# Performance work log

Measured on AMD Instinct MI355X. Metric: run time of the kernel, lower is better.

The kernel has to match this reference:

```python
import jax, jax.numpy as jnp
import numpy as np

D_MODEL = 768
NUM_HEADS = 12
NUM_REG = 4
EPS = 1e-5


def _layernorm(x, g, b):
    mu = jnp.mean(x, axis=-1, keepdims=True)
    var = jnp.mean(jnp.square(x - mu), axis=-1, keepdims=True)
    return (x - mu) * jax.lax.rsqrt(var + EPS) * g + b


def _make_mask(seq_len):
    # True = masked (disallowed), matching torch attn_mask bool semantics.
    r1 = 1 + NUM_REG
    mask = np.ones((seq_len, seq_len), dtype=bool)
    mask[0, :] = False                      # context token attends to all
    mask[1:r1, :] = False                   # register tokens attend to all
    mask[r1:, :r1] = False                  # (not use_input_context_token) == False
    mask[r1:, r1:] = ~np.eye(seq_len - r1, dtype=bool)  # feature tokens: self only
    return jnp.asarray(mask)


def setup_inputs() -> dict:
    key = jax.random.key(0)
    ks = jax.random.split(key, 16)
    B, C, H, W = 8, D_MODEL, 32, 32
    d = D_MODEL
    s = 0.02
    inp = {
        "x": jax.random.normal(ks[0], (B, C, H, W), jnp.float32),
        "context_token": jax.random.normal(ks[1], (B, 1, d), jnp.float32),
        "register_tokens": jax.random.normal(ks[2], (B, NUM_REG, d), jnp.float32),
        "in_proj_w": jax.random.normal(ks[3], (3 * d, d), jnp.float32) * s,
        "in_proj_b": jnp.zeros((3 * d,), jnp.float32),
        "out_w": jax.random.normal(ks[4], (d, d), jnp.float32) * s,
        "out_b": jnp.zeros((d,), jnp.float32),
        "ln1_g": jnp.ones((d,), jnp.float32),
        "ln1_b": jnp.zeros((d,), jnp.float32),
        "ln2_g": jnp.ones((d,), jnp.float32),
        "ln2_b": jnp.zeros((d,), jnp.float32),
        "w1": jax.random.normal(ks[5], (4 * d, d), jnp.float32) * s,
        "b1": jnp.zeros((4 * d,), jnp.float32),
        "w2": jax.random.normal(ks[6], (d, 4 * d), jnp.float32) * s,
        "b2": jnp.zeros((d,), jnp.float32),
    }
    return inp


def reference(x, context_token, register_tokens, in_proj_w, in_proj_b,
              out_w, out_b, ln1_g, ln1_b, ln2_g, ln2_b, w1, b1, w2, b2):
    B, C, H, W = x.shape
    d, nh = D_MODEL, NUM_HEADS
    hd = d // nh
    x_flat = x.reshape(B, C, H * W).transpose(0, 2, 1)          # [B, HW, d]
    tokens = jnp.concatenate([context_token, register_tokens], axis=1)
    xw = _layernorm(jnp.concatenate([tokens, x_flat], axis=1), ln1_g, ln1_b)  # [B, S, d]
    S = xw.shape[1]

    qkv = xw @ in_proj_w.T + in_proj_b                           # [B, S, 3d]
    q, k, v = jnp.split(qkv, 3, axis=-1)
    q = q.reshape(B, S, nh, hd).transpose(0, 2, 1, 3)            # [B, nh, S, hd]
    k = k.reshape(B, S, nh, hd).transpose(0, 2, 1, 3)
    v = v.reshape(B, S, nh, hd).transpose(0, 2, 1, 3)

    scores = jnp.einsum("bhqd,bhkd->bhqk", q, k) / jnp.sqrt(jnp.float32(hd))
    mask = _make_mask(S)
    scores = jnp.where(mask, jnp.float32(-1e9), scores)
    probs = jax.nn.softmax(scores, axis=-1)
    attn = jnp.einsum("bhqk,bhkd->bhqd", probs, v)               # [B, nh, S, hd]
    attn = attn.transpose(0, 2, 1, 3).reshape(B, S, d)
    attn = attn @ out_w.T + out_b

    h1 = attn + xw                                                # residual
    ff = _layernorm(h1, ln2_g, ln2_b)
    ff = jax.nn.gelu(ff @ w1.T + b1, approximate=False) @ w2.T + b2
    out = ff + h1                                                 # [B, S, d]

    r1 = 1 + NUM_REG
    ctx_out = out[:, 0:1, :]
    reg_out = out[:, 1:r1, :]
    feat_out = out[:, r1:, :].transpose(0, 2, 1).reshape(B, C, H, W)
    return feat_out, ctx_out, reg_out
```

## Files before the change

kernel.cpp:

```cpp
#include <hip/hip_runtime.h>
#include <math.h>
#include <stdint.h>

#define SEQ 1029
#define BATCH 8
#define M_TOT (BATCH * SEQ)
#define M_PAD 8320
#define NCHUNK 17

typedef float floatx4 __attribute__((ext_vector_type(4)));
typedef __bf16 bf16x8 __attribute__((ext_vector_type(8)));

__device__ __forceinline__ unsigned short f2bf(float f) {
  union { float f; unsigned u; } v; v.f = f;
  unsigned r = v.u + 0x7fffu + ((v.u >> 16) & 1u);
  return (unsigned short)(r >> 16);
}
__device__ __forceinline__ float bf2f(unsigned short h) {
  union { unsigned u; float f; } v; v.u = ((unsigned)h) << 16;
  return v.f;
}
__device__ __forceinline__ float bf_lo(unsigned u) { union { unsigned x; float f; } v; v.x = u << 16; return v.f; }
__device__ __forceinline__ float bf_hi(unsigned u) { union { unsigned x; float f; } v; v.x = u & 0xffff0000u; return v.f; }

__device__ __forceinline__ float wave_sum(float v) {
#pragma unroll
  for (int off = 32; off > 0; off >>= 1) v += __shfl_xor(v, off, 64);
  return v;
}
__device__ __forceinline__ float wave_max(float v) {
#pragma unroll
  for (int off = 32; off > 0; off >>= 1) v = fmaxf(v, __shfl_xor(v, off, 64));
  return v;
}

__device__ __forceinline__ void gload16(const unsigned short* g, unsigned short* l) {
  __builtin_amdgcn_global_load_lds(
      (const __attribute__((address_space(1))) unsigned int*)g,
      (__attribute__((address_space(3))) unsigned int*)l, 16, 0, 0);
}

#define NQ_QKV 442368
#define NQ_OUT 147456
#define NQ_W1  589824
#define NQ_W2  589824
#define NQ_PAD 8448
__global__ void convert_all(const float4* __restrict__ inw, const float4* __restrict__ outw,
                            const float4* __restrict__ w1, const float4* __restrict__ w2,
                            ushort4* __restrict__ wqkv, ushort4* __restrict__ wout,
                            ushort4* __restrict__ w1b, ushort4* __restrict__ w2b,
                            ushort4* __restrict__ xw_pad, ushort4* __restrict__ attn_pad) {
  const int i = blockIdx.x * 256 + threadIdx.x;
  const float4* src; ushort4* dst; int off;
  if (i < NQ_QKV) { src = inw; dst = wqkv; off = i; }
  else if (i < NQ_QKV + NQ_OUT) { src = outw; dst = wout; off = i - NQ_QKV; }
  else if (i < NQ_QKV + NQ_OUT + NQ_W1) { src = w1; dst = w1b; off = i - NQ_QKV - NQ_OUT; }
  else if (i < NQ_QKV + NQ_OUT + NQ_W1 + NQ_W2) { src = w2; dst = w2b; off = i - NQ_QKV - NQ_OUT - NQ_W1; }
  else {
    const int j = i - (NQ_QKV + NQ_OUT + NQ_W1 + NQ_W2);
    const ushort4 z = {0, 0, 0, 0};
    if (j < NQ_PAD) { xw_pad[j] = z; attn_pad[j] = z; }
    return;
  }
  const float4 v = src[off];
  ushort4 o;
  o.x = f2bf(v.x); o.y = f2bf(v.y); o.z = f2bf(v.z); o.w = f2bf(v.w);
  dst[off] = o;
}
#define NQ_ALL (NQ_QKV + NQ_OUT + NQ_W1 + NQ_W2 + NQ_PAD)

__global__ __launch_bounds__(256) void ln1_feat(const float* __restrict__ x,
                                                const float* __restrict__ g,
                                                const float* __restrict__ bta,
                                                unsigned short* __restrict__ xw) {
  __shared__ float tile[768 * 17];
  const int b = blockIdx.y;
  const int hw0 = blockIdx.x * 16;
  const int t = threadIdx.x;
  const float* xb = x + (size_t)b * 768 * 1024;
  const int cl = t >> 4, hl = t & 15;
  for (int it = 0; it < 48; it++) {
    const int c = it * 16 + cl;
    tile[c * 17 + hl] = xb[(size_t)c * 1024 + hw0 + hl];
  }
  __syncthreads();
  const int wave = t >> 6, lane = t & 63;
  for (int tk = wave; tk < 16; tk += 4) {
    float vals[12], s = 0.f, ss = 0.f;
#pragma unroll
    for (int i = 0; i < 12; i++) {
      const float v = tile[(lane + 64 * i) * 17 + tk];
      vals[i] = v; s += v; ss += v * v;
    }
    s = wave_sum(s); ss = wave_sum(ss);
    const float mu = s * (1.0f / 768.0f);
    const float var = ss * (1.0f / 768.0f) - mu * mu;
    const float rs = rsqrtf(var + 1e-5f);
    const int row = b * SEQ + 5 + hw0 + tk;
    unsigned short* orow = xw + (size_t)row * 768;
#pragma unroll
    for (int i = 0; i < 12; i++) {
      const int c = lane + 64 * i;
      orow[c] = f2bf((vals[i] - mu) * rs * g[c] + bta[c]);
    }
  }
}

__global__ __launch_bounds__(256) void ln1_special(const float* __restrict__ ctx,
                                                   const float* __restrict__ regs,
                                                   const float* __restrict__ g,
                                                   const float* __restrict__ bta,
                                                   unsigned short* __restrict__ xw) {
  const int gw = blockIdx.x * 4 + (threadIdx.x >> 6);
  const int lane = threadIdx.x & 63;
  if (gw >= 40) return;
  const int b = gw / 5, s = gw % 5;
  const float* src = (s == 0) ? (ctx + (size_t)b * 768)
                              : (regs + ((size_t)b * 4 + (s - 1)) * 768);
  float vals[12], sm = 0.f, ss = 0.f;
#pragma unroll
  for (int i = 0; i < 12; i++) {
    const float v = src[lane + 64 * i];
    vals[i] = v; sm += v; ss += v * v;
  }
  sm = wave_sum(sm); ss = wave_sum(ss);
  const float mu = sm * (1.0f / 768.0f);
  const float var = ss * (1.0f / 768.0f) - mu * mu;
  const float rs = rsqrtf(var + 1e-5f);
  unsigned short* orow = xw + (size_t)(b * SEQ + s) * 768;
#pragma unroll
  for (int i = 0; i < 12; i++) {
    const int c = lane + 64 * i;
    orow[c] = f2bf((vals[i] - mu) * rs * g[c] + bta[c]);
  }
}

#define BM 128
#define BN 128
#define BK 32

template <int EPI, int K, int N>
__global__ __launch_bounds__(256, 4) void gemm_bt(const unsigned short* __restrict__ A,
                                                  const unsigned short* __restrict__ W,
                                                  const float* __restrict__ bias,
                                                  const unsigned short* __restrict__ residb,
                                                  const float* __restrict__ residf,
                                                  float* __restrict__ outf,
                                                  unsigned short* __restrict__ outb) {
  __shared__ alignas(16) unsigned short As[2][BM * BK];
  __shared__ alignas(16) unsigned short Ws[2][BN * BK];
  const int t = threadIdx.x;
  const int wave = t >> 6, lane = t & 63;
  const int quad = lane >> 4, l16 = lane & 15;
  const int wm = (wave & 1) * 64, wn = (wave >> 1) * 64;
  const int tileM = blockIdx.y * BM, tileN = blockIdx.x * BN;

  const int rl = lane >> 2;
  const int kc8 = ((lane & 3) ^ ((rl >> 1) & 3)) * 8;
  const unsigned short* Ag = A + (size_t)(tileM + wave * 16 + rl) * K;
  const unsigned short* Wg = W + (size_t)(tileN + wave * 16 + rl) * K;
  const int ldst = wave * 512 + lane * 8;

  const int koff = ((quad ^ ((l16 >> 1) & 3)) * 8);

  const floatx4 zero4 = {0.f, 0.f, 0.f, 0.f};
  floatx4 acc[4][4];
#pragma unroll
  for (int i = 0; i < 4; i++)
#pragma unroll
    for (int j = 0; j < 4; j++) acc[i][j] = zero4;

  auto dma = [&](int k0, int buf) {
    gload16(Ag + k0 + kc8, &As[buf][0] + ldst);
    gload16(Ag + (size_t)64 * K + k0 + kc8, &As[buf][0] + ldst + 2048);
    gload16(Wg + k0 + kc8, &Ws[buf][0] + ldst);
    gload16(Wg + (size_t)64 * K + k0 + kc8, &Ws[buf][0] + ldst + 2048);
  };
  auto compute = [&](int buf) {
    bf16x8 af[4], wf[4];
#pragma unroll
    for (int i = 0; i < 4; i++)
      af[i] = *(const bf16x8*)(&As[buf][0] + (wm + i * 16 + l16) * BK + koff);
#pragma unroll
    for (int j = 0; j < 4; j++)
      wf[j] = *(const bf16x8*)(&Ws[buf][0] + (wn + j * 16 + l16) * BK + koff);
#pragma unroll
    for (int i = 0; i < 4; i++)
#pragma unroll
      for (int j = 0; j < 4; j++)
        acc[i][j] = __builtin_amdgcn_mfma_f32_16x16x32_bf16(af[i], wf[j], acc[i][j], 0, 0, 0);
  };

  dma(0, 0);
#pragma unroll 1
  for (int k0 = 0; k0 < K; k0 += 2 * BK) {
    __syncthreads();
    if (k0 + BK < K) dma(k0 + BK, 1);
    compute(0);
    __syncthreads();
    if (k0 + 2 * BK < K) dma(k0 + 2 * BK, 0);
    compute(1);
  }

#pragma unroll
  for (int i = 0; i < 4; i++) {
    const int mbase = tileM + wm + i * 16 + quad * 4;
#pragma unroll
    for (int j = 0; j < 4; j++) {
      const int n = tileN + wn + j * 16 + l16;
      const float bv = bias[n];
#pragma unroll
      for (int r = 0; r < 4; r++) {
        const size_t idx = (size_t)(mbase + r) * N + n;
        float v = acc[i][j][r] + bv;
        if constexpr (EPI == 0) {
          outb[idx] = f2bf(v);
        } else if constexpr (EPI == 1) {
          outf[idx] = v + bf2f(residb[idx]);
        } else if constexpr (EPI == 2) {
          v = 0.5f * v * (1.0f + erff(v * 0.70710678118654752f));
          outb[idx] = f2bf(v);
        } else {
          outf[idx] = v + residf[idx];
        }
      }
    }
  }
}

__global__ __launch_bounds__(256) void attn_feat(const unsigned short* __restrict__ qkv,
                                                 unsigned short* __restrict__ attn) {
  __shared__ float kk[5][64];
  __shared__ float vv[5][64];
  const int b = blockIdx.z, h = blockIdx.y;
  const int t = threadIdx.x;
  const size_t base = (size_t)b * SEQ;
  for (int i = t; i < 320; i += 256) {
    const int j = i >> 6, dd = i & 63;
    const size_t rb = (base + j) * 2304 + (size_t)h * 64 + dd;
    kk[j][dd] = bf2f(qkv[rb + 768]);
    vv[j][dd] = bf2f(qkv[rb + 1536]);
  }
  __syncthreads();
  const int wave = t >> 6, lane = t & 63;
  const int s = 5 + blockIdx.x * 4 + wave;
  const size_t row = (base + s) * 2304 + (size_t)h * 64;
  const float q = bf2f(qkv[row + lane]);
  const float kself = bf2f(qkv[row + 768 + lane]);
  const float vself = bf2f(qkv[row + 1536 + lane]);
  float sc[6];
#pragma unroll
  for (int j = 0; j < 5; j++) sc[j] = wave_sum(q * kk[j][lane]) * 0.125f;
  sc[5] = wave_sum(q * kself) * 0.125f;
  float mx = sc[0];
#pragma unroll
  for (int j = 1; j < 6; j++) mx = fmaxf(mx, sc[j]);
  float den = 0.f, e[6];
#pragma unroll
  for (int j = 0; j < 6; j++) { e[j] = expf(sc[j] - mx); den += e[j]; }
  const float inv = 1.0f / den;
  float o = 0.f;
#pragma unroll
  for (int j = 0; j < 5; j++) o += e[j] * vv[j][lane];
  o += e[5] * vself;
  attn[(base + s) * 768 + (size_t)h * 64 + lane] = f2bf(o * inv);
}

__global__ __launch_bounds__(256) void attn_part(const unsigned short* __restrict__ qkv,
                                                 float* __restrict__ part) {
  __shared__ float qs[5][64];
  __shared__ float sc[5][64];
  __shared__ float mArr[5], lArr[5];
  __shared__ float og[4][320];
  const int c = blockIdx.x, h = blockIdx.y, b = blockIdx.z;
  const int t = threadIdx.x;
  const size_t base = (size_t)b * SEQ;
  const int kbase = (c < 16) ? (5 + 64 * c) : 0;
  const int nvalid = (c < 16) ? 64 : 5;

  for (int i = t; i < 320; i += 256)
    qs[i >> 6][i & 63] = bf2f(qkv[(base + (i >> 6)) * 2304 + (size_t)h * 64 + (i & 63)]);
  __syncthreads();

  const int keyloc = t >> 2, dc = t & 3;
  const int key = kbase + keyloc;
  const unsigned short* krow = qkv + (base + key) * 2304 + 768 + (size_t)h * 64;
  const uint4 k0 = *(const uint4*)(krow + dc * 8);
  const uint4 k1 = *(const uint4*)(krow + dc * 8 + 32);
  float kf[16];
  {
    const unsigned ku[8] = {k0.x, k0.y, k0.z, k0.w, k1.x, k1.y, k1.z, k1.w};
#pragma unroll
    for (int j = 0; j < 8; j++) { kf[2 * j] = bf_lo(ku[j]); kf[2 * j + 1] = bf_hi(ku[j]); }
  }
#pragma unroll
  for (int q = 0; q < 5; q++) {
    const float* qp = qs[q];
    float d0 = 0.f;
#pragma unroll
    for (int j = 0; j < 8; j++) d0 += qp[dc * 8 + j] * kf[j];
#pragma unroll
    for (int j = 0; j < 8; j++) d0 += qp[dc * 8 + 32 + j] * kf[8 + j];
    d0 += __shfl_xor(d0, 1, 64);
    d0 += __shfl_xor(d0, 2, 64);
    if (dc == 0) sc[q][keyloc] = (keyloc < nvalid) ? d0 * 0.125f : -1e30f;
  }
  __syncthreads();

  const int wave = t >> 6, lane = t & 63;
  for (int q = wave; q < 5; q += 4) {
    const float v = sc[q][lane];
    const float m = wave_max(v);
    const float e = expf(v - m);
    sc[q][lane] = e;
    const float l = wave_sum(e);
    if (lane == 0) { mArr[q] = m; lArr[q] = l; }
  }
  __syncthreads();

  const int d = t & 63, g = t >> 6;
  float o[5] = {0.f, 0.f, 0.f, 0.f, 0.f};
  for (int i = 0; i < 16; i++) {
    const int kl = g * 16 + i;
    const float v = bf2f(qkv[(base + kbase + kl) * 2304 + 1536 + (size_t)h * 64 + d]);
#pragma unroll
    for (int q = 0; q < 5; q++) o[q] += sc[q][kl] * v;
  }
#pragma unroll
  for (int q = 0; q < 5; q++) og[g][q * 64 + d] = o[q];
  __syncthreads();

  float* pw = part + (size_t)((b * 12 + h) * NCHUNK + c) * 5 * 66;
  for (int i = t; i < 320; i += 256) {
    const int q = i >> 6, dd = i & 63;
    pw[q * 66 + 2 + dd] = og[0][i] + og[1][i] + og[2][i] + og[3][i];
    if (dd == 0) { pw[q * 66] = mArr[q]; pw[q * 66 + 1] = lArr[q]; }
  }
}

__global__ __launch_bounds__(64) void attn_comb(const float* __restrict__ part,
                                                unsigned short* __restrict__ attn) {
  const int qi = blockIdx.x, h = blockIdx.y, b = blockIdx.z;
  const int d = threadIdx.x;
  float M = -3e38f, L = 0.f, o = 0.f;
  for (int c = 0; c < NCHUNK; c++) {
    const float* p = part + ((size_t)((b * 12 + h) * NCHUNK + c) * 5 + qi) * 66;
    const float mc = p[0], lc = p[1], oc = p[2 + d];
    if (mc > M) {
      const float s = expf(M - mc);
      L = L * s + lc; o = o * s + oc; M = mc;
    } else {
      const float w = expf(mc - M);
      L += lc * w; o += oc * w;
    }
  }
  attn[((size_t)b * SEQ + qi) * 768 + (size_t)h * 64 + d] = f2bf(o / L);
}

__global__ __launch_bounds__(256) void ln2_kernel(const float* __restrict__ h1,
                                                  const float* __restrict__ g,
                                                  const float* __restrict__ bta,
                                                  unsigned short* __restrict__ out) {
  const int row = blockIdx.x * 4 + (threadIdx.x >> 6);
  const int lane = threadIdx.x & 63;
  const float* r = h1 + (size_t)row * 768;
  float vals[12], sm = 0.f, ss = 0.f;
#pragma unroll
  for (int i = 0; i < 12; i++) {
    const float v = r[lane + 64 * i];
    vals[i] = v; sm += v; ss += v * v;
  }
  sm = wave_sum(sm); ss = wave_sum(ss);
  const float mu = sm * (1.0f / 768.0f);
  const float var = ss * (1.0f / 768.0f) - mu * mu;
  const float rs = rsqrtf(var + 1e-5f);
  unsigned short* orow = out + (size_t)row * 768;
#pragma unroll
  for (int i = 0; i < 12; i++) {
    const int c = lane + 64 * i;
    orow[c] = f2bf((vals[i] - mu) * rs * g[c] + bta[c]);
  }
}

__global__ __launch_bounds__(256) void scatter_all(const float* __restrict__ outb,
                                                   float* __restrict__ dout) {
  const int t = threadIdx.x;
  const int b = blockIdx.z;
  if (blockIdx.x == 24) {
    const int i = (b * 32 + blockIdx.y) * 256 + t;
    if (i >= 40 * 768) return;
    const int rowi = i / 768, c = i % 768;
    const int bb = rowi / 5, s = rowi % 5;
    const float v = outb[(size_t)(bb * SEQ + s) * 768 + c];
    if (s == 0) dout[6291456 + (size_t)bb * 768 + c] = v;
    else dout[6291456 + 6144 + ((size_t)bb * 4 + (s - 1)) * 768 + c] = v;
    return;
  }
  __shared__ float tl[32][33];
  const int hw0 = blockIdx.y * 32, c0 = blockIdx.x * 32;
  const int i = t >> 5, j = t & 31;
#pragma unroll
  for (int r = 0; r < 4; r++) {
    const int hwi = i + r * 8;
    tl[hwi][j] = outb[(size_t)(b * SEQ + 5 + hw0 + hwi) * 768 + c0 + j];
  }
  __syncthreads();
#pragma unroll
  for (int r = 0; r < 4; r++) {
    const int ci = i + r * 8;
    dout[(size_t)b * 768 * 1024 + (size_t)(c0 + ci) * 1024 + hw0 + j] = tl[j][ci];
  }
}

extern "C" void kernel_launch(void* const* d_in, const int* in_sizes, int n_in,
                              void* d_out, int out_size, void* d_ws, size_t ws_size,
                              hipStream_t stream) {
  const float* x    = (const float*)d_in[0];
  const float* ctx  = (const float*)d_in[1];
  const float* regs = (const float*)d_in[2];
  const float* inw  = (const float*)d_in[3];
  const float* inb  = (const float*)d_in[4];
  const float* outw = (const float*)d_in[5];
  const float* outbi= (const float*)d_in[6];
  const float* ln1g = (const float*)d_in[7];
  const float* ln1b = (const float*)d_in[8];
  const float* ln2g = (const float*)d_in[9];
  const float* ln2b = (const float*)d_in[10];
  const float* w1   = (const float*)d_in[11];
  const float* b1   = (const float*)d_in[12];
  const float* w2   = (const float*)d_in[13];
  const float* b2   = (const float*)d_in[14];

  char* ws = (char*)d_ws;
  unsigned short* wqkv_b = (unsigned short*)(ws + 0);
  unsigned short* wout_b = (unsigned short*)(ws + 3538944);
  unsigned short* w1_b   = (unsigned short*)(ws + 4718592);
  unsigned short* w2_b   = (unsigned short*)(ws + 9437184);
  unsigned short* xw_b   = (unsigned short*)(ws + 14155776);
  unsigned short* ln2o_b = (unsigned short*)(ws + 26935296);
  float*          h1_f   = (float*)(ws + 39714816);
  unsigned short* qkv_b  = (unsigned short*)(ws + 65273856);
  unsigned short* attn_b = (unsigned short*)(ws + 103612416);
  float*          out_f  = (float*)(ws + 14155776);
  unsigned short* ffm_b  = (unsigned short*)(ws + 65273856);
  float*          part_f = (float*)(ws + 39714816);
  float* dout = (float*)d_out;

  convert_all<<<(NQ_ALL + 255) / 256, 256, 0, stream>>>(
      (const float4*)inw, (const float4*)outw, (const float4*)w1, (const float4*)w2,
      (ushort4*)wqkv_b, (ushort4*)wout_b, (ushort4*)w1_b, (ushort4*)w2_b,
      (ushort4*)(xw_b + (size_t)M_TOT * 768), (ushort4*)(attn_b + (size_t)M_TOT * 768));

  ln1_feat<<<dim3(64, 8), 256, 0, stream>>>(x, ln1g, ln1b, xw_b);
  ln1_special<<<10, 256, 0, stream>>>(ctx, regs, ln1g, ln1b, xw_b);

  gemm_bt<0, 768, 2304><<<dim3(2304 / BN, M_PAD / BM), 256, 0, stream>>>(
      xw_b, wqkv_b, inb, nullptr, nullptr, nullptr, qkv_b);

  attn_feat<<<dim3(256, 12, 8), 256, 0, stream>>>(qkv_b, attn_b);
  attn_part<<<dim3(NCHUNK, 12, 8), 256, 0, stream>>>(qkv_b, part_f);
  attn_comb<<<dim3(5, 12, 8), 64, 0, stream>>>(part_f, attn_b);

  gemm_bt<1, 768, 768><<<dim3(768 / BN, M_PAD / BM), 256, 0, stream>>>(
      attn_b, wout_b, outbi, xw_b, nullptr, h1_f, nullptr);

  ln2_kernel<<<M_PAD / 4, 256, 0, stream>>>(h1_f, ln2g, ln2b, ln2o_b);

  gemm_bt<2, 768, 3072><<<dim3(3072 / BN, M_PAD / BM), 256, 0, stream>>>(
      ln2o_b, w1_b, b1, nullptr, nullptr, nullptr, ffm_b);

  gemm_bt<3, 3072, 768><<<dim3(768 / BN, M_PAD / BM), 256, 0, stream>>>(
      ffm_b, w2_b, b2, nullptr, h1_f, out_f, nullptr);

  scatter_all<<<dim3(25, 32, 8), 256, 0, stream>>>(out_f, dout);
}
```

Before: 430.3 us.

## Deepen GEMM LDS pipeline to 3-4 buffers and remap tiles per XCD

```diff
diff --git a/kernel.cpp b/kernel.cpp
--- a/kernel.cpp
+++ b/kernel.cpp
@@ -38,6 +38,13 @@
   __builtin_amdgcn_global_load_lds(
       (const __attribute__((address_space(1))) unsigned int*)g,
       (__attribute__((address_space(3))) unsigned int*)l, 16, 0, 0);
+}
+
+template <int C>
+__device__ __forceinline__ void vwait() {
+  if constexpr (C == 0) asm volatile("s_waitcnt vmcnt(0)" ::: "memory");
+  else if constexpr (C == 4) asm volatile("s_waitcnt vmcnt(4)" ::: "memory");
+  else asm volatile("s_waitcnt vmcnt(8)" ::: "memory");
 }
 
 #define NQ_QKV 442368
@@ -139,21 +146,30 @@
 #define BN 128
 #define BK 32
 
-template <int EPI, int K, int N>
-__global__ __launch_bounds__(256, 4) void gemm_bt(const unsigned short* __restrict__ A,
-                                                  const unsigned short* __restrict__ W,
-                                                  const float* __restrict__ bias,
-                                                  const unsigned short* __restrict__ residb,
-                                                  const float* __restrict__ residf,
-                                                  float* __restrict__ outf,
-                                                  unsigned short* __restrict__ outb) {
-  __shared__ alignas(16) unsigned short As[2][BM * BK];
-  __shared__ alignas(16) unsigned short Ws[2][BN * BK];
+template <int EPI, int K, int N, int NBUF>
+__global__ __launch_bounds__(256, NBUF == 3 ? 3 : 2) void gemm_bt(
+    const unsigned short* __restrict__ A,
+    const unsigned short* __restrict__ W,
+    const float* __restrict__ bias,
+    const unsigned short* __restrict__ residb,
+    const float* __restrict__ residf,
+    float* __restrict__ outf,
+    unsigned short* __restrict__ outb) {
+  __shared__ alignas(16) unsigned short As[NBUF][BM * BK];
+  __shared__ alignas(16) unsigned short Ws[NBUF][BN * BK];
   const int t = threadIdx.x;
   const int wave = t >> 6, lane = t & 63;
   const int quad = lane >> 4, l16 = lane & 15;
   const int wm = (wave & 1) * 64, wn = (wave >> 1) * 64;
-  const int tileM = blockIdx.y * BM, tileN = blockIdx.x * BN;
+
+  constexpr int GX = N / BN;
+  constexpr int NWG = GX * (M_PAD / BM);
+  constexpr int Q8 = NWG / 8, R8 = NWG % 8;
+  const int flat = blockIdx.y * GX + blockIdx.x;
+  const int xcd = flat & 7, idx = flat >> 3;
+  const int wgid = (xcd < R8 ? xcd * (Q8 + 1) : R8 * (Q8 + 1) + (xcd - R8) * Q8) + idx;
+  const int tileM = (wgid / GX) * BM;
+  const int tileN = (wgid % GX) * BN;
 
   const int rl = lane >> 2;
   const int kc8 = ((lane & 3) ^ ((rl >> 1) & 3)) * 8;
@@ -191,16 +207,31 @@
         acc[i][j] = __builtin_amdgcn_mfma_f32_16x16x32_bf16(af[i], wf[j], acc[i][j], 0, 0, 0);
   };
 
-  dma(0, 0);
+  constexpr int NSTEP = K / BK;
+  constexpr int PF = NBUF - 1;
+
+#pragma unroll
+  for (int p = 0; p < PF; ++p) dma(p * BK, p);
+
+  int cb = 0, db = PF % NBUF;
 #pragma unroll 1
-  for (int k0 = 0; k0 < K; k0 += 2 * BK) {
-    __syncthreads();
-    if (k0 + BK < K) dma(k0 + BK, 1);
-    compute(0);
-    __syncthreads();
-    if (k0 + 2 * BK < K) dma(k0 + 2 * BK, 0);
-    compute(1);
-  }
+  for (int i = 0; i < NSTEP - PF; ++i) {
+    vwait<4 * (NBUF - 2)>();
+    __builtin_amdgcn_s_barrier();
+    __builtin_amdgcn_sched_barrier(0);
+    dma((i + PF) * BK, db);
+    db = (db + 1 == NBUF) ? 0 : db + 1;
+    compute(cb);
+    cb = (cb + 1 == NBUF) ? 0 : cb + 1;
+  }
+  if constexpr (NBUF == 4) {
+    vwait<8>(); __builtin_amdgcn_s_barrier(); __builtin_amdgcn_sched_barrier(0);
+    compute(cb); cb = (cb + 1 == NBUF) ? 0 : cb + 1;
+  }
+  vwait<4>(); __builtin_amdgcn_s_barrier(); __builtin_amdgcn_sched_barrier(0);
+  compute(cb); cb = (cb + 1 == NBUF) ? 0 : cb + 1;
+  vwait<0>(); __builtin_amdgcn_s_barrier(); __builtin_amdgcn_sched_barrier(0);
+  compute(cb);
 
 #pragma unroll
   for (int i = 0; i < 4; i++) {
@@ -211,17 +242,17 @@
       const float bv = bias[n];
 #pragma unroll
       for (int r = 0; r < 4; r++) {
-        const size_t idx = (size_t)(mbase + r) * N + n;
+        const size_t idx2 = (size_t)(mbase + r) * N + n;
         float v = acc[i][j][r] + bv;
         if constexpr (EPI == 0) {
-          outb[idx] = f2bf(v);
+          outb[idx2] = f2bf(v);
         } else if constexpr (EPI == 1) {
-          outf[idx] = v + bf2f(residb[idx]);
+          outf[idx2] = v + bf2f(residb[idx2]);
         } else if constexpr (EPI == 2) {
           v = 0.5f * v * (1.0f + erff(v * 0.70710678118654752f));
-          outb[idx] = f2bf(v);
+          outb[idx2] = f2bf(v);
         } else {
-          outf[idx] = v + residf[idx];
+          outf[idx2] = v + residf[idx2];
         }
       }
     }
@@ -454,22 +485,22 @@
   ln1_feat<<<dim3(64, 8), 256, 0, stream>>>(x, ln1g, ln1b, xw_b);
   ln1_special<<<10, 256, 0, stream>>>(ctx, regs, ln1g, ln1b, xw_b);
 
-  gemm_bt<0, 768, 2304><<<dim3(2304 / BN, M_PAD / BM), 256, 0, stream>>>(
+  gemm_bt<0, 768, 2304, 3><<<dim3(2304 / BN, M_PAD / BM), 256, 0, stream>>>(
       xw_b, wqkv_b, inb, nullptr, nullptr, nullptr, qkv_b);
 
   attn_feat<<<dim3(256, 12, 8), 256, 0, stream>>>(qkv_b, attn_b);
   attn_part<<<dim3(NCHUNK, 12, 8), 256, 0, stream>>>(qkv_b, part_f);
   attn_comb<<<dim3(5, 12, 8), 64, 0, stream>>>(part_f, attn_b);
 
-  gemm_bt<1, 768, 768><<<dim3(768 / BN, M_PAD / BM), 256, 0, stream>>>(
+  gemm_bt<1, 768, 768, 4><<<dim3(768 / BN, M_PAD / BM), 256, 0, stream>>>(
       attn_b, wout_b, outbi, xw_b, nullptr, h1_f, nullptr);
 
   ln2_kernel<<<M_PAD / 4, 256, 0, stream>>>(h1_f, ln2g, ln2b, ln2o_b);
 
-  gemm_bt<2, 768, 3072><<<dim3(3072 / BN, M_PAD / BM), 256, 0, stream>>>(
+  gemm_bt<2, 768, 3072, 3><<<dim3(3072 / BN, M_PAD / BM), 256, 0, stream>>>(
       ln2o_b, w1_b, b1, nullptr, nullptr, nullptr, ffm_b);
 
-  gemm_bt<3, 3072, 768><<<dim3(768 / BN, M_PAD / BM), 256, 0, stream>>>(
+  gemm_bt<3, 3072, 768, 4><<<dim3(768 / BN, M_PAD / BM), 256, 0, stream>>>(
       ffm_b, w2_b, b2, nullptr, h1_f, out_f, nullptr);
 
   scatter_all<<<dim3(25, 32, 8), 256, 0, stream>>>(out_f, dout);
```

Measured after the change: 419.6 us. 1.03x faster.
